# Performance work log

Hardware: AMD Instinct MI355X
Metric: run time of the kernel (lower is better)

Reference implementation:

```python
import jax, jax.numpy as jnp
import numpy as np

NUM_SUBSET = 3
BN_EPS = 1e-5
T_CONST = 40
NUM_HEADS = 8


def _unit_gcn(x, PA, Wa, ba, Wb, bb, Wd, bd, gamma, beta):
    # x: (B, C, T, V). 1x1 convs become channel einsums. flag=True, GMPool_G,
    # num_point not in {3,7} -> adjacency A = PA only. down = identity (C_in==C_out).
    B, C, T, V = x.shape
    inter = Wa.shape[1]
    x_flat = x.reshape(B, C * T, V)
    y = None
    for i in range(NUM_SUBSET):
        a = jnp.einsum('bctv,ic->bitv', x, Wa[i]) + ba[i][None, :, None, None]
        A1 = a.transpose(0, 3, 1, 2).reshape(B, V, inter * T)          # (B, V, inter*T)
        b = jnp.einsum('bctv,ic->bitv', x, Wb[i]) + bb[i][None, :, None, None]
        A2 = b.reshape(B, inter * T, V)                                 # (B, inter*T, V)
        S = jax.nn.softmax((A1 @ A2) / (inter * T), axis=-2) + PA[i]    # (B, V, V), Softmax(-2)
        z = (x_flat @ S).reshape(B, C, T, V)
        z = jnp.einsum('bctv,oc->botv', z, Wd[i]) + bd[i][None, :, None, None]
        y = z if y is None else y + z
    # BatchNorm2d (eval: running_mean=0, running_var=1)
    y = y * (gamma / jnp.sqrt(1.0 + BN_EPS))[None, :, None, None] + beta[None, :, None, None]
    y = y + x  # residual via identity down-path
    return jax.nn.relu(y)


def _mab_forward(Q, K, fck, fcv, fco):
    B, Npt, DK = K.shape
    T = T_CONST
    C = DK // T
    Kr = K.transpose(0, 2, 1).reshape(B, C, T, Npt)   # (B, C, T, V)
    Kg = _unit_gcn(Kr, *fck)
    Vg = _unit_gcn(Kr, *fcv)
    Kf = Kg.transpose(0, 3, 1, 2).reshape(B, Npt, -1)  # (B, V, C*T)
    Vf = Vg.transpose(0, 3, 1, 2).reshape(B, Npt, -1)
    S, DV = Q.shape[1], Q.shape[2]
    ds = DV // NUM_HEADS
    Qh = Q.reshape(B, S, NUM_HEADS, ds)
    Kh = Kf.reshape(B, Npt, NUM_HEADS, ds)
    Vh = Vf.reshape(B, Npt, NUM_HEADS, ds)
    scores = jnp.einsum('bqhd,bkhd->bhqk', Qh, Kh) / jnp.sqrt(jnp.float32(DV))
    attn = jax.nn.softmax(scores, axis=-1)  # softmax_dim=2 of (H*B, S, V) == last axis
    Oh = Qh + jnp.einsum('bhqk,bkhd->bqhd', attn, Vh)
    O = Oh.reshape(B, S, DV)  # cat over heads along feature dim == reshape
    Og = O.transpose(0, 2, 1).reshape(B, C, T, S)
    Og = _unit_gcn(Og, *fco)
    Og = Og.transpose(0, 3, 1, 2).reshape(B, S, -1)
    return O + jax.nn.relu(Og)


def setup_inputs() -> dict:
    key = jax.random.key(0)
    ks = jax.random.split(key, 8)
    B, Npt, Sd, T, C, inter = 256, 25, 10, 40, 64, 16
    D = C * T  # 2560

    def gcn_params(kk, V):
        k = jax.random.split(kk, 5)
        return dict(
            PA=jnp.full((3, V, V), 1e-6, jnp.float32),
            Wa=jax.random.normal(k[0], (3, inter, C), jnp.float32) * np.float32(np.sqrt(2.0 / C)),
            ba=jnp.zeros((3, inter), jnp.float32),
            Wb=jax.random.normal(k[1], (3, inter, C), jnp.float32) * np.float32(np.sqrt(2.0 / C)),
            bb=jnp.zeros((3, inter), jnp.float32),
            Wd=jax.random.normal(k[2], (3, C, C), jnp.float32) * np.float32(np.sqrt(2.0 / (3 * C))),
            bd=jnp.zeros((3, C), jnp.float32),
            gamma=jax.random.uniform(k[3], (C,), jnp.float32, 0.5, 1.5),
            beta=jax.random.normal(k[4], (C,), jnp.float32) * 0.01,
        )

    inp = {
        'Q': jax.random.normal(ks[0], (B, Sd, D), jnp.float32),
        'K': jax.random.normal(ks[1], (B, Npt, D), jnp.float32),
    }
    for pref, kk, V in (('fck', ks[2], Npt), ('fcv', ks[3], Npt), ('fco', ks[4], Sd)):
        for n, v in gcn_params(kk, V).items():
            inp[pref + '_' + n] = v
    for n in ('relrec_s1', 'relsend_s1', 'relrec_s2', 'relsend_s2', 'relrec_speed', 'relsend_speed'):
        inp[n] = jnp.zeros((1,), jnp.int32)  # unused (branch only active for V==7, T==20)
    return inp


def reference(Q, K,
              fck_PA, fck_Wa, fck_ba, fck_Wb, fck_bb, fck_Wd, fck_bd, fck_gamma, fck_beta,
              fcv_PA, fcv_Wa, fcv_ba, fcv_Wb, fcv_bb, fcv_Wd, fcv_bd, fcv_gamma, fcv_beta,
              fco_PA, fco_Wa, fco_ba, fco_Wb, fco_bb, fco_Wd, fco_bd, fco_gamma, fco_beta,
              relrec_s1, relsend_s1, relrec_s2, relsend_s2, relrec_speed, relsend_speed):
    fck = (fck_PA, fck_Wa, fck_ba, fck_Wb, fck_bb, fck_Wd, fck_bd, fck_gamma, fck_beta)
    fcv = (fcv_PA, fcv_Wa, fcv_ba, fcv_Wb, fcv_bb, fcv_Wd, fcv_bd, fcv_gamma, fcv_beta)
    fco = (fco_PA, fco_Wa, fco_ba, fco_Wb, fco_bb, fco_Wd, fco_bd, fco_gamma, fco_beta)
    return _mab_forward(Q, K, fck, fcv, fco)
```

## Files before the change

### kernel.cpp

```cpp
#include <hip/hip_runtime.h>
#include <hip/hip_bf16.h>

#define BB 256
#define CC 64
#define TT 40
#define DD 2560
#define V1 25
#define V2 10
#define INTER 16
#define NH 8
#define DSH 320
#define HSLAB 8000

typedef __hip_bfloat16 bf16;
typedef unsigned int uint;
typedef unsigned short ushort;
typedef __attribute__((ext_vector_type(8))) short bf16x8;
typedef __attribute__((ext_vector_type(4))) float f32x4;

__device__ __forceinline__ float b2f(bf16 x) { return __bfloat162float(x); }

__device__ __forceinline__ ushort f2bb(float f) {
    uint x = __float_as_uint(f);
    uint r = x + 0x7fffu + ((x >> 16) & 1u);
    return (ushort)(r >> 16);
}
__device__ __forceinline__ float blo(uint u) { return __uint_as_float(u << 16); }
__device__ __forceinline__ float bhi(uint u) { return __uint_as_float(u & 0xffff0000u); }
__device__ __forceinline__ float b2f_us(ushort h) { return __uint_as_float(((uint)h) << 16); }
__device__ __forceinline__ uint4 pack8(const float* a) {
    uint4 pk;
    pk.x = (uint)f2bb(a[0]) | ((uint)f2bb(a[1]) << 16);
    pk.y = (uint)f2bb(a[2]) | ((uint)f2bb(a[3]) << 16);
    pk.z = (uint)f2bb(a[4]) | ((uint)f2bb(a[5]) << 16);
    pk.w = (uint)f2bb(a[6]) | ((uint)f2bb(a[7]) << 16);
    return pk;
}

__device__ __forceinline__ int swz64(int row, int col) {
    return row * 64 + ((((col >> 3) ^ row) & 7) << 3) + (col & 7);
}
__device__ __forceinline__ int swzC(int c, int col) {
    return c * 128 + ((((col >> 3) ^ c) & 15) << 3) + (col & 7);
}

__global__ __launch_bounds__(256) void prep_wabf(
    const float* __restrict__ Wa0, const float* __restrict__ Wb0,
    const float* __restrict__ Wa1, const float* __restrict__ Wb1,
    ushort* __restrict__ Wabf) {
    const int tid = threadIdx.x;
    for (int e = tid; e < 768; e += 256) {
        const int lane = e & 63, mat = (e >> 6) & 3, s = e >> 8;
        const int ln = lane & 15, lq = lane >> 4;
        const float* Wp = (mat == 0) ? Wa0 : (mat == 1) ? Wb0 : (mat == 2) ? Wa1 : Wb1;
        const float* src = Wp + s * 1024 + ln * 64 + lq * 8;
        ushort* dst = Wabf + e * 16;
        #pragma unroll
        for (int i = 0; i < 8; ++i) {
            dst[i] = f2bb(src[i]);
            dst[8 + i] = f2bb(src[32 + i]);
        }
    }
}

__global__ __launch_bounds__(512) void gcn_S3(
    const float* __restrict__ X,
    const ushort* __restrict__ Wabf,
    const float* __restrict__ ba0, const float* __restrict__ bb0,
    const float* __restrict__ ba1, const float* __restrict__ bb1,
    bf16* __restrict__ Xw, float* __restrict__ Mpart) {
    __shared__ ushort xsT[208][72];
    __shared__ ushort abT[4][32][136];
    __shared__ float biasS3[192];

    const int tid = threadIdx.x;
    const int b = blockIdx.x & 255, tc = blockIdx.x >> 8;
    const int t0 = tc * 8;
    const int lane = tid & 63, w = tid >> 6;
    const int ln = lane & 15, lq = lane >> 4;
    const int mat = w & 3, half = w >> 2;

    const float* Xb = X + (size_t)b * V1 * DD;
    for (int e = tid; e < V1 * 64; e += 512) {
        const int v = e >> 6, c = e & 63;
        const float* src = Xb + (size_t)v * DD + c * TT + t0;
        const float4 f0 = *(const float4*)src;
        const float4 f1 = *(const float4*)(src + 4);
        const float tmp[8] = {f0.x, f0.y, f0.z, f0.w, f1.x, f1.y, f1.z, f1.w};
        #pragma unroll
        for (int tl = 0; tl < 8; ++tl) xsT[v * 8 + tl][c] = f2bb(tmp[tl]);
    }
    if (tid < 192) {
        const int s = tid >> 6, m2 = (tid >> 4) & 3, j = tid & 15;
        const float* bp = (m2 == 0) ? ba0 : (m2 == 1) ? bb0 : (m2 == 2) ? ba1 : bb1;
        biasS3[tid] = bp[s * 16 + j];
    }
    __syncthreads();

    for (int e = tid; e < 1600; e += 512) {
        const int v = e >> 6, h = (e >> 3) & 7, tl = e & 7;
        *(uint4*)(Xw + (size_t)(b * NH + h) * HSLAB + v * 320 + (t0 + tl) * 8) =
            *(const uint4*)&xsT[v * 8 + tl][h * 8];
    }

    for (int s = 0; s < 3; ++s) {
        const ushort* wp = Wabf + (((s * 4 + mat) * 64 + lane) << 4);
        union { uint4 u; bf16x8 v; } ua, ub;
        ua.u = *(const uint4*)wp;
        ub.u = *(const uint4*)(wp + 8);
        float br[4];
        #pragma unroll
        for (int r = 0; r < 4; ++r) br[r] = biasS3[s * 64 + mat * 16 + lq * 4 + r];

        if (s) __syncthreads();

        const int ntEnd = half ? 13 : 7;
        for (int nt = half ? 7 : 0; nt < ntEnd; ++nt) {
            const bf16x8 b0 = *(const bf16x8*)&xsT[nt * 16 + ln][lq * 8];
            const bf16x8 b1 = *(const bf16x8*)&xsT[nt * 16 + ln][lq * 8 + 32];
            f32x4 acc = (f32x4){0.f, 0.f, 0.f, 0.f};
            acc = __builtin_amdgcn_mfma_f32_16x16x32_bf16(ua.v, b0, acc, 0, 0, 0);
            acc = __builtin_amdgcn_mfma_f32_16x16x32_bf16(ub.v, b1, acc, 0, 0, 0);
            const int p = nt * 16 + ln;
            if (p < 200) {
                const int v = p >> 3, tl = p & 7;
                #pragma unroll
                for (int r = 0; r < 4; ++r)
                    abT[mat][v][(lq * 4 + r) * 8 + tl] = f2bb(acc[r] + br[r]);
            }
        }
        __syncthreads();

        {
            const int np = w >> 2, mt = (w >> 1) & 1, ntl = w & 1;
            const ushort* Ap = &abT[np * 2 + 0][mt * 16 + ln][lq * 8];
            const ushort* Bp = &abT[np * 2 + 1][ntl * 16 + ln][lq * 8];
            f32x4 g = (f32x4){0.f, 0.f, 0.f, 0.f};
            g = __builtin_amdgcn_mfma_f32_16x16x32_bf16(
                    *(const bf16x8*)Ap, *(const bf16x8*)Bp, g, 0, 0, 0);
            g = __builtin_amdgcn_mfma_f32_16x16x32_bf16(
                    *(const bf16x8*)(Ap + 32), *(const bf16x8*)(Bp + 32), g, 0, 0, 0);
            g = __builtin_amdgcn_mfma_f32_16x16x32_bf16(
                    *(const bf16x8*)(Ap + 64), *(const bf16x8*)(Bp + 64), g, 0, 0, 0);
            g = __builtin_amdgcn_mfma_f32_16x16x32_bf16(
                    *(const bf16x8*)(Ap + 96), *(const bf16x8*)(Bp + 96), g, 0, 0, 0);
            const int vp = ntl * 16 + ln;
            if (vp < V1) {
                float* Mb = Mpart + (((size_t)tc * 256 + b) * 6 + (s * 2 + np)) * 625;
                #pragma unroll
                for (int r = 0; r < 4; ++r) {
                    const int v = mt * 16 + lq * 4 + r;
                    if (v < V1) Mb[v * V1 + vp] = g[r];
                }
            }
        }
    }
}

__global__ __launch_bounds__(128) void reduce_softmax(
    const float* __restrict__ Mpart,
    const float* __restrict__ PA0, const float* __restrict__ PA1,
    const float* __restrict__ WdK, const float* __restrict__ WdV,
    ushort* __restrict__ Sbf, ushort* __restrict__ Wdf) {
    __shared__ float Ms[625];
    const int tid = threadIdx.x, b = blockIdx.x, snp = blockIdx.y;
    const int s = snp >> 1, np = snp & 1;

    if (b == 0) {
        for (int e = tid; e < 256; e += 128) {
            const int wv = e >> 6, l = e & 63;
            const int lnn = l & 15, lqq = l >> 4;
            const float* Wp = (np ? WdV : WdK) + s * 4096 + (wv * 16 + lnn) * 64 + lqq * 8;
            ushort* dst = Wdf + (((np * 3 + s) * 4 + wv) * 64 + l) * 16;
            #pragma unroll
            for (int j = 0; j < 8; ++j) {
                dst[j] = f2bb(Wp[j]);
                dst[8 + j] = f2bb(Wp[32 + j]);
            }
        }
    }

    for (int e = tid; e < 625; e += 128) {
        float sum = 0.f;
        #pragma unroll
        for (int tcc = 0; tcc < 5; ++tcc)
            sum += Mpart[(((size_t)tcc * 256 + b) * 6 + snp) * 625 + e];
        Ms[e] = sum;
    }
    __syncthreads();
    if (tid < 32) {
        ushort* SbfRow = Sbf + ((((size_t)b * 2 + np) * 3 + s) << 10) + tid * 32;
        if (tid < V1) {
            const int vp = tid;
            const float invIT = 1.0f / 640.0f;
            float mx = -1e30f;
            for (int v = 0; v < V1; ++v) mx = fmaxf(mx, Ms[v * V1 + vp]);
            float sum = 0.f;
            for (int v = 0; v < V1; ++v) sum += expf((Ms[v * V1 + vp] - mx) * invIT);
            const float rs = 1.f / sum;
            const float* PAn = np ? PA1 : PA0;
            for (int v = 0; v < V1; ++v) {
                const float e_ = expf((Ms[v * V1 + vp] - mx) * invIT);
                SbfRow[v] = f2bb(e_ * rs + PAn[(s * V1 + v) * V1 + vp]);
            }
            for (int v = V1; v < 32; ++v) SbfRow[v] = 0;
        } else {
            for (int v = 0; v < 32; ++v) SbfRow[v] = 0;
        }
    }
}

__global__ __launch_bounds__(256) void gcn_S2O(
    const float* __restrict__ X,
    const float* __restrict__ Wa0, const float* __restrict__ ba0,
    const float* __restrict__ Wb0, const float* __restrict__ bb0,
    const float* __restrict__ PA0, const float* __restrict__ WdO,
    ushort* __restrict__ SbfO, ushort* __restrict__ Wdf3) {
    constexpr int V = V2;
    constexpr int P = 80;
    __shared__ ushort xs[64][P];
    __shared__ ushort ab[32][P];
    __shared__ ushort wT[64][32];
    __shared__ float biasL[32];
    __shared__ float M[100];

    const int tid = threadIdx.x, b = blockIdx.x, s = blockIdx.y;

    if (b == 0) {
        const int e = tid;
        if (e < 256) {
            const int wv = e >> 6, l = e & 63;
            const int lnn = l & 15, lqq = l >> 4;
            const float* Wp = WdO + s * 4096 + (wv * 16 + lnn) * 64 + lqq * 8;
            ushort* dst = Wdf3 + (((s * 4 + wv) * 64 + l) << 4);
            #pragma unroll
            for (int j = 0; j < 8; ++j) {
                dst[j] = f2bb(Wp[j]);
                dst[8 + j] = f2bb(Wp[32 + j]);
            }
        }
    }

    for (int e = tid; e < 16 * 64; e += 256) {
        int c = e & 63, j = e >> 6;
        wT[c][j]      = f2bb(Wa0[s * 1024 + e]);
        wT[c][16 + j] = f2bb(Wb0[s * 1024 + e]);
    }
    if (tid < 16) {
        biasL[tid]      = ba0[s * 16 + tid];
        biasL[16 + tid] = bb0[s * 16 + tid];
    }

    float macc = 0.f;

    const float* Xb = X + (size_t)b * V * DD;
    for (int tc = 0; tc < 5; ++tc) {
        const int t0 = tc * 8;
        for (int e = tid; e < V * 64; e += 256) {
            const int v = e >> 6, c = e & 63;
            const float* src = Xb + (size_t)v * DD + c * TT + t0;
            const float4 f0 = *(const float4*)src;
            const float4 f1 = *(const float4*)(src + 4);
            const float tmp[8] = {f0.x, f0.y, f0.z, f0.w, f1.x, f1.y, f1.z, f1.w};
            *(uint4*)&xs[c][v * 8] = pack8(tmp);
        }
        __syncthreads();
        for (int tau = tid; tau < 80; tau += 256) {
            const int rq = tau % 8, co = tau / 8;
            float acc[4][8];
            #pragma unroll
            for (int r = 0; r < 4; ++r) {
                const float bv = biasL[4 * rq + r];
                #pragma unroll
                for (int cc = 0; cc < 8; ++cc) acc[r][cc] = bv;
            }
            for (int c = 0; c < 64; ++c) {
                const uint2 wv = *(const uint2*)&wT[c][4 * rq];
                const uint4 xv = *(const uint4*)&xs[c][8 * co];
                const float w0 = blo(wv.x), w1 = bhi(wv.x);
                const float w2 = blo(wv.y), w3 = bhi(wv.y);
                const float x0 = blo(xv.x), x1 = bhi(xv.x);
                const float x2 = blo(xv.y), x3 = bhi(xv.y);
                const float x4 = blo(xv.z), x5 = bhi(xv.z);
                const float x6 = blo(xv.w), x7 = bhi(xv.w);
                acc[0][0] += w0 * x0; acc[0][1] += w0 * x1;
                acc[0][2] += w0 * x2; acc[0][3] += w0 * x3;
                acc[0][4] += w0 * x4; acc[0][5] += w0 * x5;
                acc[0][6] += w0 * x6; acc[0][7] += w0 * x7;
                acc[1][0] += w1 * x0; acc[1][1] += w1 * x1;
                acc[1][2] += w1 * x2; acc[1][3] += w1 * x3;
                acc[1][4] += w1 * x4; acc[1][5] += w1 * x5;
                acc[1][6] += w1 * x6; acc[1][7] += w1 * x7;
                acc[2][0] += w2 * x0; acc[2][1] += w2 * x1;
                acc[2][2] += w2 * x2; acc[2][3] += w2 * x3;
                acc[2][4] += w2 * x4; acc[2][5] += w2 * x5;
                acc[2][6] += w2 * x6; acc[2][7] += w2 * x7;
                acc[3][0] += w3 * x0; acc[3][1] += w3 * x1;
                acc[3][2] += w3 * x2; acc[3][3] += w3 * x3;
                acc[3][4] += w3 * x4; acc[3][5] += w3 * x5;
                acc[3][6] += w3 * x6; acc[3][7] += w3 * x7;
            }
            #pragma unroll
            for (int r = 0; r < 4; ++r)
                *(uint4*)&ab[4 * rq + r][8 * co] = pack8(acc[r]);
        }
        __syncthreads();
        if (tid < 100) {
            const int v = tid / V, vp = tid % V;
            float mm = 0.f;
            #pragma unroll
            for (int j = 0; j < 16; ++j) {
                const uint4 av = *(const uint4*)&ab[j][v * 8];
                const uint4 bv = *(const uint4*)&ab[16 + j][vp * 8];
                mm += blo(av.x) * blo(bv.x) + bhi(av.x) * bhi(bv.x)
                    + blo(av.y) * blo(bv.y) + bhi(av.y) * bhi(bv.y)
                    + blo(av.z) * blo(bv.z) + bhi(av.z) * bhi(bv.z)
                    + blo(av.w) * blo(bv.w) + bhi(av.w) * bhi(bv.w);
            }
            macc += mm;
        }
    }

    if (tid < 100) M[tid] = macc;
    __syncthreads();

    const float invIT = 1.0f / 640.0f;
    if (tid < 16) {
        ushort* So = SbfO + ((size_t)b * 3 + s) * 256 + tid * 16;
        if (tid < V) {
            const int vp = tid;
            float mx = -1e30f;
            for (int v = 0; v < V; ++v) mx = fmaxf(mx, M[v * V + vp]);
            float sum = 0.f;
            for (int v = 0; v < V; ++v) sum += expf((M[v * V + vp] - mx) * invIT);
            const float rs = 1.f / sum;
            for (int v = 0; v < V; ++v) {
                const float e_ = expf((M[v * V + vp] - mx) * invIT);
                So[v] = f2bb(e_ * rs + PA0[(s * V + v) * V + vp]);
            }
            for (int v = V; v < 16; ++v) So[v] = 0;
        } else {
            for (int v = 0; v < 16; ++v) So[v] = 0;
        }
    }
}

__global__ __launch_bounds__(256) void gcn_applyKV(
    const bf16* __restrict__ Xbf,
    const ushort* __restrict__ Sbf, const ushort* __restrict__ Wdf,
    const float* __restrict__ bdK, const float* __restrict__ gK, const float* __restrict__ beK,
    const float* __restrict__ bdV, const float* __restrict__ gV, const float* __restrict__ beV,
    bf16* __restrict__ Kg, bf16* __restrict__ Vg) {

    __shared__ ushort xsT[100 * 64];
    __shared__ ushort SlTs[6144];
    __shared__ ushort uC[8192];
    __shared__ float bias6[6 * 64];

    const int tid = threadIdx.x, b = blockIdx.x, chunk = blockIdx.y;
    const int lane = tid & 63, w = tid >> 6;
    const int ln = lane & 15, lq = lane >> 4;
    const int t0 = chunk * 4;

    if (tid < 64) {
        bias6[tid]       = bdK[tid] + bdK[64 + tid] + bdK[128 + tid];
        bias6[64 + tid]  = bdV[tid] + bdV[64 + tid] + bdV[128 + tid];
        bias6[128 + tid] = gK[tid] * rsqrtf(1.f + 1e-5f);
        bias6[192 + tid] = gV[tid] * rsqrtf(1.f + 1e-5f);
        bias6[256 + tid] = beK[tid];
        bias6[320 + tid] = beV[tid];
    }
    const bf16* Xb = Xbf + (size_t)b * NH * HSLAB;
    for (int e = tid; e < 1024; e += 256) {
        const int h = e >> 7, v = (e >> 2) & 31, tl = e & 3;
        if (v < V1)
            *(uint4*)&xsT[swz64(v * 4 + tl, h * 8)] =
                *(const uint4*)(Xb + (size_t)h * HSLAB + v * 320 + (t0 + tl) * 8);
    }
    {
        const ushort* Sb = Sbf + (size_t)b * 6144;
        for (int e = tid; e < 768; e += 256)
            ((uint4*)SlTs)[e] = ((const uint4*)Sb)[e];
    }
    __syncthreads();

    {
        const int c = lane, q = w;
        #pragma unroll
        for (int j = 0; j < 4; ++j) {
            ushort vals[8];
            #pragma unroll
            for (int i = 0; i < 8; ++i) {
                const int v0 = q * 8 + i;
                vals[i] = (v0 < V1) ? xsT[swz64(v0 * 4 + j, c)] : (ushort)0;
            }
            uint4 pk;
            pk.x = (uint)vals[0] | ((uint)vals[1] << 16);
            pk.y = (uint)vals[2] | ((uint)vals[3] << 16);
            pk.z = (uint)vals[4] | ((uint)vals[5] << 16);
            pk.w = (uint)vals[6] | ((uint)vals[7] << 16);
            *(uint4*)&uC[swzC(c, j * 32 + q * 8)] = pk;
        }
    }
    __syncthreads();

    bf16x8 aF[4];
    #pragma unroll
    for (int tl = 0; tl < 4; ++tl)
        aF[tl] = *(const bf16x8*)&uC[swzC(w * 16 + ln, tl * 32 + lq * 8)];
    __syncthreads();

    for (int g = 0; g < 2; ++g) {
        f32x4 acc[7];
        #pragma unroll
        for (int tn = 0; tn < 7; ++tn) acc[tn] = (f32x4){0.f, 0.f, 0.f, 0.f};

        for (int s = 0; s < 3; ++s) {
            const ushort* wp = Wdf + ((((g * 3 + s) * 4 + w) * 64 + lane) << 4);
            union { uint4 u; bf16x8 v; } ua, ub;
            ua.u = *(const uint4*)wp;
            ub.u = *(const uint4*)(wp + 8);

            if (g | s) __syncthreads();

            #pragma unroll
            for (int nt = 0; nt < 2; ++nt) {
                const bf16x8 bF =
                    *(const bf16x8*)&SlTs[((g * 3 + s) << 10) + (nt * 16 + ln) * 32 + lq * 8];
                const int v = nt * 16 + ln;
                #pragma unroll
                for (int tl = 0; tl < 4; ++tl) {
                    f32x4 d = (f32x4){0.f, 0.f, 0.f, 0.f};
                    d = __builtin_amdgcn_mfma_f32_16x16x32_bf16(aF[tl], bF, d, 0, 0, 0);
                    if (v < V1) {
                        uint2 pk;
                        pk.x = (uint)f2bb(d[0]) | ((uint)f2bb(d[1]) << 16);
                        pk.y = (uint)f2bb(d[2]) | ((uint)f2bb(d[3]) << 16);
                        *(uint2*)&uC[swz64(v * 4 + tl, w * 16 + lq * 4)] = pk;
                    }
                }
            }
            __syncthreads();

            #pragma unroll
            for (int tn = 0; tn < 7; ++tn) {
                const bf16x8 b0 = *(const bf16x8*)&uC[swz64(tn * 16 + ln, lq * 8)];
                const bf16x8 b1 = *(const bf16x8*)&uC[swz64(tn * 16 + ln, lq * 8 + 32)];
                acc[tn] = __builtin_amdgcn_mfma_f32_16x16x32_bf16(ua.v, b0, acc[tn], 0, 0, 0);
                acc[tn] = __builtin_amdgcn_mfma_f32_16x16x32_bf16(ub.v, b1, acc[tn], 0, 0, 0);
            }
        }
        __syncthreads();

        {
            const int c0 = w * 16 + lq * 4;
            float bb[4], ss[4], be[4];
            #pragma unroll
            for (int r = 0; r < 4; ++r) {
                bb[r] = bias6[g * 64 + c0 + r];
                ss[r] = bias6[128 + g * 64 + c0 + r];
                be[r] = bias6[256 + g * 64 + c0 + r];
            }
            #pragma unroll
            for (int tn = 0; tn < 7; ++tn) {
                const int p = tn * 16 + ln;
                if (p < 100) {
                    const uint2 u = *(const uint2*)&xsT[swz64(p, c0)];
                    const float rs[4] = {blo(u.x), bhi(u.x), blo(u.y), bhi(u.y)};
                    float y[4];
                    #pragma unroll
                    for (int r = 0; r < 4; ++r)
                        y[r] = fmaxf((acc[tn][r] + bb[r]) * ss[r] + be[r] + rs[r], 0.f);
                    uint2 pk;
                    pk.x = (uint)f2bb(y[0]) | ((uint)f2bb(y[1]) << 16);
                    pk.y = (uint)f2bb(y[2]) | ((uint)f2bb(y[3]) << 16);
                    *(uint2*)&uC[swz64(p, c0)] = pk;
                }
            }
        }
        __syncthreads();

        bf16* outp = (g ? Vg : Kg) + (size_t)b * NH * HSLAB;
        for (int e = tid; e < 1024; e += 256) {
            const int h = e >> 7, v = (e >> 2) & 31, tl = e & 3;
            if (v < V1)
                *(uint4*)(outp + (size_t)h * HSLAB + v * 320 + (t0 + tl) * 8) =
                    *(const uint4*)&uC[swz64(v * 4 + tl, h * 8)];
        }
    }
}

__global__ __launch_bounds__(256) void gcn_applyO(
    const float* __restrict__ X,
    const ushort* __restrict__ SbfO, const ushort* __restrict__ Wdf3,
    const float* __restrict__ bdO, const float* __restrict__ gO, const float* __restrict__ beO,
    float* __restrict__ out_f, const float* __restrict__ Obuf) {

    __shared__ ushort xsT[80 * 64];
    __shared__ ushort uC[8192];
    __shared__ ushort SlTs16[832];
    __shared__ float bias3[3 * 64];

    const int tid = threadIdx.x, b = blockIdx.x, chunk = blockIdx.y;
    const int lane = tid & 63, w = tid >> 6;
    const int ln = lane & 15, lq = lane >> 4;
    const int t0 = chunk * 8;

    if (tid < 64) {
        bias3[tid]       = bdO[tid] + bdO[64 + tid] + bdO[128 + tid];
        bias3[64 + tid]  = gO[tid] * rsqrtf(1.f + 1e-5f);
        bias3[128 + tid] = beO[tid];
    }
    const float* Xb = X + (size_t)b * V2 * DD;
    for (int e = tid; e < 640; e += 256) {
        const int v = e >> 6, c = e & 63;
        const float* src = Xb + (size_t)v * DD + c * TT + t0;
        const float4 f0 = *(const float4*)src;
        const float4 f1 = *(const float4*)(src + 4);
        const float tmp[8] = {f0.x, f0.y, f0.z, f0.w, f1.x, f1.y, f1.z, f1.w};
        #pragma unroll
        for (int tl = 0; tl < 8; ++tl) xsT[swz64(v * 8 + tl, c)] = f2bb(tmp[tl]);
    }
    {
        const uint4* Sb = (const uint4*)(SbfO + (size_t)b * 768);
        for (int e = tid; e < 96; e += 256) ((uint4*)SlTs16)[e] = Sb[e];
    }
    __syncthreads();

    {
        const int c = lane;
        #pragma unroll
        for (int jj = 0; jj < 4; ++jj) {
            const int u_ = w * 4 + jj;
            const int tl = u_ >> 1, q = u_ & 1;
            ushort vals[8];
            #pragma unroll
            for (int i = 0; i < 8; ++i) {
                const int v0 = q * 8 + i;
                vals[i] = (v0 < V2) ? xsT[swz64(v0 * 8 + tl, c)] : (ushort)0;
            }
            uint4 pk;
            pk.x = (uint)vals[0] | ((uint)vals[1] << 16);
            pk.y = (uint)vals[2] | ((uint)vals[3] << 16);
            pk.z = (uint)vals[4] | ((uint)vals[5] << 16);
            pk.w = (uint)vals[6] | ((uint)vals[7] << 16);
            *(uint4*)&uC[swzC(c, tl * 16 + q * 8)] = pk;
        }
    }
    __syncthreads();

    union { uint4 u; bf16x8 v; } z8; z8.u = (uint4){0u, 0u, 0u, 0u};
    bf16x8 aF[8];
    #pragma unroll
    for (int tl = 0; tl < 8; ++tl)
        aF[tl] = (lq < 2) ? *(const bf16x8*)&uC[swzC(w * 16 + ln, tl * 16 + lq * 8)]
                          : z8.v;
    __syncthreads();

    f32x4 acc[5];
    #pragma unroll
    for (int tn = 0; tn < 5; ++tn) acc[tn] = (f32x4){0.f, 0.f, 0.f, 0.f};

    for (int s = 0; s < 3; ++s) {
        const ushort* wp = Wdf3 + (((s * 4 + w) * 64 + lane) << 4);
        union { uint4 u; bf16x8 v; } ua, ub;
        ua.u = *(const uint4*)wp;
        ub.u = *(const uint4*)(wp + 8);

        if (s) __syncthreads();

        const bf16x8 bF = (lq < 2)
            ? *(const bf16x8*)&SlTs16[s * 256 + ln * 16 + lq * 8] : z8.v;
        #pragma unroll
        for (int tl = 0; tl < 8; ++tl) {
            f32x4 d = (f32x4){0.f, 0.f, 0.f, 0.f};
            d = __builtin_amdgcn_mfma_f32_16x16x32_bf16(aF[tl], bF, d, 0, 0, 0);
            if (ln < V2) {
                uint2 pk;
                pk.x = (uint)f2bb(d[0]) | ((uint)f2bb(d[1]) << 16);
                pk.y = (uint)f2bb(d[2]) | ((uint)f2bb(d[3]) << 16);
                *(uint2*)&uC[swz64(ln * 8 + tl, w * 16 + lq * 4)] = pk;
            }
        }
        __syncthreads();

        #pragma unroll
        for (int tn = 0; tn < 5; ++tn) {
            const bf16x8 b0 = *(const bf16x8*)&uC[swz64(tn * 16 + ln, lq * 8)];
            const bf16x8 b1 = *(const bf16x8*)&uC[swz64(tn * 16 + ln, lq * 8 + 32)];
            acc[tn] = __builtin_amdgcn_mfma_f32_16x16x32_bf16(ua.v, b0, acc[tn], 0, 0, 0);
            acc[tn] = __builtin_amdgcn_mfma_f32_16x16x32_bf16(ub.v, b1, acc[tn], 0, 0, 0);
        }
    }
    __syncthreads();

    {
        const int c0 = w * 16 + lq * 4;
        float bb[4], ss[4], be[4];
        #pragma unroll
        for (int r = 0; r < 4; ++r) {
            bb[r] = bias3[c0 + r];
            ss[r] = bias3[64 + c0 + r];
            be[r] = bias3[128 + c0 + r];
        }
        #pragma unroll
        for (int tn = 0; tn < 5; ++tn) {
            const int p = tn * 16 + ln;
            const uint2 u = *(const uint2*)&xsT[swz64(p, c0)];
            const float rs[4] = {blo(u.x), bhi(u.x), blo(u.y), bhi(u.y)};
            float y[4];
            #pragma unroll
            for (int r = 0; r < 4; ++r)
                y[r] = fmaxf((acc[tn][r] + bb[r]) * ss[r] + be[r] + rs[r], 0.f);
            uint2 pk;
            pk.x = (uint)f2bb(y[0]) | ((uint)f2bb(y[1]) << 16);
            pk.y = (uint)f2bb(y[2]) | ((uint)f2bb(y[3]) << 16);
            *(uint2*)&uC[swz64(p, c0)] = pk;
        }
    }
    __syncthreads();

    {
        const int v = tid & 15, ci = tid >> 4;
        if (v < V2) {
            #pragma unroll
            for (int r = 0; r < 4; ++r) {
                const int c = ci * 4 + r;
                const size_t base = (size_t)b * V2 * DD + (size_t)v * DD + c * TT + t0;
                const float4 o0 = *(const float4*)&Obuf[base];
                const float4 o1 = *(const float4*)&Obuf[base + 4];
                float4 y0, y1;
                y0.x = o0.x + b2f_us(uC[swz64(v * 8 + 0, c)]);
                y0.y = o0.y + b2f_us(uC[swz64(v * 8 + 1, c)]);
                y0.z = o0.z + b2f_us(uC[swz64(v * 8 + 2, c)]);
                y0.w = o0.w + b2f_us(uC[swz64(v * 8 + 3, c)]);
                y1.x = o1.x + b2f_us(uC[swz64(v * 8 + 4, c)]);
                y1.y = o1.y + b2f_us(uC[swz64(v * 8 + 5, c)]);
                y1.z = o1.z + b2f_us(uC[swz64(v * 8 + 6, c)]);
                y1.w = o1.w + b2f_us(uC[swz64(v * 8 + 7, c)]);
                *(float4*)&out_f[base] = y0;
                *(float4*)&out_f[base + 4] = y1;
            }
        }
    }
}

__global__ __launch_bounds__(256) void attn_kernel(const float* __restrict__ Q,
                                                   const bf16* __restrict__ Kg,
                                                   const bf16* __restrict__ Vg,
                                                   float* __restrict__ O) {
    int b = blockIdx.x, h = blockIdx.y, tid = threadIdx.x;
    __shared__ float qs[10 * DSH];
    __shared__ float ks[V1 * 321];
    __shared__ float att[10 * V1];
    const float* Qb = Q + (size_t)b * 10 * DD + h * DSH;
    for (int e = tid; e < 10 * DSH; e += 256) {
        int q = e / DSH, d = e % DSH;
        qs[e] = Qb[(size_t)q * DD + d];
    }
    const bf16* Kb = Kg + (size_t)(b * NH + h) * HSLAB;
    for (int e = tid; e < V1 * TT; e += 256) {
        const int kk = e / TT, t = e % TT;
        const uint4 u = *(const uint4*)(Kb + (size_t)e * 8);
        const ushort* us = (const ushort*)&u;
        float* dst = &ks[kk * 321 + t];
        #pragma unroll
        for (int cl = 0; cl < 8; ++cl) dst[cl * 40] = b2f_us(us[cl]);
    }
    __syncthreads();
    const float scale = 0.019764235376052370f;
    for (int e = tid; e < 10 * V1; e += 256) {
        int q = e / V1, kk = e % V1;
        float acc = 0.f;
        #pragma unroll 8
        for (int d = 0; d < DSH; ++d) acc += qs[q * DSH + d] * ks[kk * 321 + d];
        att[e] = acc * scale;
    }
    __syncthreads();
    if (tid < 10) {
        float mx = -1e30f;
        for (int k = 0; k < V1; ++k) mx = fmaxf(mx, att[tid * V1 + k]);
        float sum = 0.f;
        for (int k = 0; k < V1; ++k) {
            float e_ = expf(att[tid * V1 + k] - mx);
            att[tid * V1 + k] = e_;
            sum += e_;
        }
        float r = 1.0f / sum;
        for (int k = 0; k < V1; ++k) att[tid * V1 + k] *= r;
    }
    const bf16* Vb = Vg + (size_t)(b * NH + h) * HSLAB;
    for (int e = tid; e < V1 * TT; e += 256) {
        const int kk = e / TT, t = e % TT;
        const uint4 u = *(const uint4*)(Vb + (size_t)e * 8);
        const ushort* us = (const ushort*)&u;
        float* dst = &ks[kk * 321 + t];
        #pragma unroll
        for (int cl = 0; cl < 8; ++cl) dst[cl * 40] = b2f_us(us[cl]);
    }
    __syncthreads();
    float* Ob = O + (size_t)b * 10 * DD + h * DSH;
    for (int e = tid; e < 10 * DSH; e += 256) {
        int q = e / DSH, dl = e % DSH;
        float acc = 0.f;
        #pragma unroll
        for (int k = 0; k < V1; ++k) acc += att[q * V1 + k] * ks[k * 321 + dl];
        Ob[(size_t)q * DD + dl] = qs[e] + acc;
    }
}

extern "C" void kernel_launch(void* const* d_in, const int* in_sizes, int n_in,
                              void* d_out, int out_size, void* d_ws, size_t ws_size,
                              hipStream_t stream) {
    const float* Q = (const float*)d_in[0];
    const float* K = (const float*)d_in[1];
    const float* fck_PA = (const float*)d_in[2];
    const float* fck_Wa = (const float*)d_in[3];
    const float* fck_ba = (const float*)d_in[4];
    const float* fck_Wb = (const float*)d_in[5];
    const float* fck_bb = (const float*)d_in[6];
    const float* fck_Wd = (const float*)d_in[7];
    const float* fck_bd = (const float*)d_in[8];
    const float* fck_gamma = (const float*)d_in[9];
    const float* fck_beta = (const float*)d_in[10];
    const float* fcv_PA = (const float*)d_in[11];
    const float* fcv_Wa = (const float*)d_in[12];
    const float* fcv_ba = (const float*)d_in[13];
    const float* fcv_Wb = (const float*)d_in[14];
    const float* fcv_bb = (const float*)d_in[15];
    const float* fcv_Wd = (const float*)d_in[16];
    const float* fcv_bd = (const float*)d_in[17];
    const float* fcv_gamma = (const float*)d_in[18];
    const float* fcv_beta = (const float*)d_in[19];
    const float* fco_PA = (const float*)d_in[20];
    const float* fco_Wa = (const float*)d_in[21];
    const float* fco_ba = (const float*)d_in[22];
    const float* fco_Wb = (const float*)d_in[23];
    const float* fco_bb = (const float*)d_in[24];
    const float* fco_Wd = (const float*)d_in[25];
    const float* fco_bd = (const float*)d_in[26];
    const float* fco_gamma = (const float*)d_in[27];
    const float* fco_beta = (const float*)d_in[28];

    char* wsb = (char*)d_ws;
    bf16* Xbf = (bf16*)(wsb);
    bf16* Vg = (bf16*)(wsb);
    bf16* Kg = (bf16*)(wsb + 32768000);
    float* Mpart = (float*)(wsb + 65536000);
    float* O = (float*)(wsb + 65536000);
    ushort* Sbf = (ushort*)(wsb + 84736000);
    ushort* Wdf = (ushort*)(wsb + 88000000);
    ushort* SbfO = (ushort*)(wsb + 32768000);
    ushort* Wdf3 = (ushort*)(wsb + 33300000);
    ushort* Wabf = (ushort*)(wsb + 95590400);

    prep_wabf<<<dim3(1), dim3(256), 0, stream>>>(
        fck_Wa, fck_Wb, fcv_Wa, fcv_Wb, Wabf);

    gcn_S3<<<dim3(BB * 5), dim3(512), 0, stream>>>(
        K, Wabf, fck_ba, fck_bb, fcv_ba, fcv_bb, Xbf, Mpart);

    reduce_softmax<<<dim3(BB, 6), dim3(128), 0, stream>>>(
        Mpart, fck_PA, fcv_PA, fck_Wd, fcv_Wd, Sbf, Wdf);

    gcn_applyKV<<<dim3(BB, 10), dim3(256), 0, stream>>>(
        Xbf, Sbf, Wdf,
        fck_bd, fck_gamma, fck_beta,
        fcv_bd, fcv_gamma, fcv_beta, Kg, Vg);

    attn_kernel<<<dim3(BB, NH), dim3(256), 0, stream>>>(Q, Kg, Vg, O);

    gcn_S2O<<<dim3(BB, 3), dim3(256), 0, stream>>>(
        O, fco_Wa, fco_ba, fco_Wb, fco_bb, fco_PA, fco_Wd, SbfO, Wdf3);

    gcn_applyO<<<dim3(BB, 5), dim3(256), 0, stream>>>(
        O, SbfO, Wdf3, fco_bd, fco_gamma, fco_beta, (float*)d_out, O);
}
```

Baseline: 446.4 us.

## Compute attention QK scores with bf16 MFMA and vectorize attention loads

Rewrites the attention kernel so the Q·K score products run on 16x16x32 bf16 MFMA instructions instead of scalar FP32 dot loops. Q is split into bf16 hi and lo parts to keep near-FP32 accuracy, and K is copied straight into a swizzled shared layout. Q loads and the attention-times-V output stage now use float4 loads and stores. This cuts scalar FMA work and shared-memory traffic in the score stage. It relies on unused padded MFMA rows and columns (Q rows 10–15, K rows 25–31) reading uninitialized shared memory that never reaches the output.

```diff
diff --git a/kernel.cpp b/kernel.cpp
--- a/kernel.cpp
+++ b/kernel.cpp
@@ -42,6 +42,10 @@
 }
 __device__ __forceinline__ int swzC(int c, int col) {
     return c * 128 + ((((col >> 3) ^ c) & 15) << 3) + (col & 7);
+}
+__device__ __forceinline__ int swz320(int row, int k) {
+    const int g = k >> 3;
+    return row * 320 + (((g & ~7) | ((g ^ row) & 7)) << 3) + (k & 7);
 }
 
 __global__ __launch_bounds__(256) void prep_wabf(
@@ -649,63 +653,106 @@
                                                    const bf16* __restrict__ Kg,
                                                    const bf16* __restrict__ Vg,
                                                    float* __restrict__ O) {
-    int b = blockIdx.x, h = blockIdx.y, tid = threadIdx.x;
-    __shared__ float qs[10 * DSH];
-    __shared__ float ks[V1 * 321];
-    __shared__ float att[10 * V1];
+    __shared__ float smA[10240];
+    __shared__ float attP[4][16][16];
+    __shared__ float attF[16][32];
+    ushort* qs2h = (ushort*)smA;
+    ushort* qs2l = (ushort*)smA + 5120;
+    ushort* ksw  = (ushort*)smA + 10240;
+    float* vbuf = smA;
+
+    const int b = blockIdx.x, h = blockIdx.y, tid = threadIdx.x;
+    const int lane = tid & 63, w = tid >> 6;
+    const int ln = lane & 15, lq = lane >> 4;
+
     const float* Qb = Q + (size_t)b * 10 * DD + h * DSH;
-    for (int e = tid; e < 10 * DSH; e += 256) {
-        int q = e / DSH, d = e % DSH;
-        qs[e] = Qb[(size_t)q * DD + d];
+    for (int e = tid; e < 800; e += 256) {
+        const int q = e / 80, seg = e % 80;
+        const int dd0 = seg * 4;
+        const float4 f = *(const float4*)(Qb + (size_t)q * DD + dd0);
+        const float ff[4] = {f.x, f.y, f.z, f.w};
+        #pragma unroll
+        for (int j = 0; j < 4; ++j) {
+            const int dd = dd0 + j;
+            const int k = (dd % 40) * 8 + dd / 40;
+            const int idx = swz320(q, k);
+            const ushort hi = f2bb(ff[j]);
+            qs2h[idx] = hi;
+            qs2l[idx] = f2bb(ff[j] - b2f_us(hi));
+        }
     }
     const bf16* Kb = Kg + (size_t)(b * NH + h) * HSLAB;
-    for (int e = tid; e < V1 * TT; e += 256) {
-        const int kk = e / TT, t = e % TT;
-        const uint4 u = *(const uint4*)(Kb + (size_t)e * 8);
-        const ushort* us = (const ushort*)&u;
-        float* dst = &ks[kk * 321 + t];
-        #pragma unroll
-        for (int cl = 0; cl < 8; ++cl) dst[cl * 40] = b2f_us(us[cl]);
-    }
-    __syncthreads();
+    for (int e = tid; e < 1000; e += 256) {
+        const int kk = e / 40, g = e % 40;
+        const int gp = (g & ~7) | ((g ^ kk) & 7);
+        *(uint4*)&ksw[kk * 320 + gp * 8] = *(const uint4*)(Kb + (size_t)e * 8);
+    }
+    __syncthreads();
+
+    {
+        const int ntl = w & 1;
+        const int ch0 = (w >> 1) * 5;
+        f32x4 d = (f32x4){0.f, 0.f, 0.f, 0.f};
+        #pragma unroll
+        for (int c5 = 0; c5 < 5; ++c5) {
+            const int k0 = (ch0 + c5) * 32 + lq * 8;
+            const bf16x8 ah = *(const bf16x8*)&qs2h[swz320(ln, k0)];
+            const bf16x8 al = *(const bf16x8*)&qs2l[swz320(ln, k0)];
+            const bf16x8 bF = *(const bf16x8*)&ksw[swz320(ntl * 16 + ln, k0)];
+            d = __builtin_amdgcn_mfma_f32_16x16x32_bf16(ah, bF, d, 0, 0, 0);
+            d = __builtin_amdgcn_mfma_f32_16x16x32_bf16(al, bF, d, 0, 0, 0);
+        }
+        #pragma unroll
+        for (int r = 0; r < 4; ++r) attP[w][lq * 4 + r][ln] = d[r];
+    }
+    __syncthreads();
+
     const float scale = 0.019764235376052370f;
-    for (int e = tid; e < 10 * V1; e += 256) {
-        int q = e / V1, kk = e % V1;
-        float acc = 0.f;
-        #pragma unroll 8
-        for (int d = 0; d < DSH; ++d) acc += qs[q * DSH + d] * ks[kk * 321 + d];
-        att[e] = acc * scale;
-    }
-    __syncthreads();
-    if (tid < 10) {
-        float mx = -1e30f;
-        for (int k = 0; k < V1; ++k) mx = fmaxf(mx, att[tid * V1 + k]);
-        float sum = 0.f;
-        for (int k = 0; k < V1; ++k) {
-            float e_ = expf(att[tid * V1 + k] - mx);
-            att[tid * V1 + k] = e_;
-            sum += e_;
-        }
-        float r = 1.0f / sum;
-        for (int k = 0; k < V1; ++k) att[tid * V1 + k] *= r;
+    for (int e = tid; e < 512; e += 256) {
+        const int q = e >> 5, kk = e & 31;
+        const int ntl = kk >> 4, kkl = kk & 15;
+        attF[q][kk] = (attP[ntl][q][kkl] + attP[ntl + 2][q][kkl]) * scale;
     }
     const bf16* Vb = Vg + (size_t)(b * NH + h) * HSLAB;
-    for (int e = tid; e < V1 * TT; e += 256) {
+    for (int e = tid; e < 1000; e += 256) {
         const int kk = e / TT, t = e % TT;
         const uint4 u = *(const uint4*)(Vb + (size_t)e * 8);
         const ushort* us = (const ushort*)&u;
-        float* dst = &ks[kk * 321 + t];
+        float* dst = &vbuf[kk * 324 + t];
         #pragma unroll
         for (int cl = 0; cl < 8; ++cl) dst[cl * 40] = b2f_us(us[cl]);
     }
     __syncthreads();
+
+    if (tid < 10) {
+        float mx = -1e30f;
+        for (int k = 0; k < V1; ++k) mx = fmaxf(mx, attF[tid][k]);
+        float sum = 0.f;
+        for (int k = 0; k < V1; ++k) {
+            float e_ = expf(attF[tid][k] - mx);
+            attF[tid][k] = e_;
+            sum += e_;
+        }
+        float r = 1.0f / sum;
+        for (int k = 0; k < V1; ++k) attF[tid][k] *= r;
+    }
+    __syncthreads();
+
     float* Ob = O + (size_t)b * 10 * DD + h * DSH;
-    for (int e = tid; e < 10 * DSH; e += 256) {
-        int q = e / DSH, dl = e % DSH;
-        float acc = 0.f;
-        #pragma unroll
-        for (int k = 0; k < V1; ++k) acc += att[q * V1 + k] * ks[k * 321 + dl];
-        Ob[(size_t)q * DD + dl] = qs[e] + acc;
+    for (int e = tid; e < 800; e += 256) {
+        const int q = e / 80, seg = e % 80;
+        const int dl0 = seg * 4;
+        float ax = 0.f, ay = 0.f, az = 0.f, aw = 0.f;
+        #pragma unroll
+        for (int kk = 0; kk < V1; ++kk) {
+            const float a = attF[q][kk];
+            const float4 v = *(const float4*)&vbuf[kk * 324 + dl0];
+            ax += a * v.x; ay += a * v.y; az += a * v.z; aw += a * v.w;
+        }
+        const float4 qv = *(const float4*)(Qb + (size_t)q * DD + dl0);
+        float4 o;
+        o.x = qv.x + ax; o.y = qv.y + ay; o.z = qv.z + az; o.w = qv.w + aw;
+        *(float4*)(Ob + (size_t)q * DD + dl0) = o;
     }
 }
 
```

After: 422.9 us. 1.06x faster.
